# Performance work log

Measured on AMD Instinct MI355X. Metric: run time of the kernel, lower is better.

## Reference

```python
import jax, jax.numpy as jnp
import numpy as np

D_MODEL = 2048
NHEAD = 16
HEAD_DIM = D_MODEL // NHEAD  # 128
B, S = 2, 2048
THETA = 10000.0


def setup_inputs() -> dict:
    key = jax.random.key(0)
    ks = jax.random.split(key, 10)
    sc = 1.0 / np.sqrt(D_MODEL)
    inp = {
        "x": jax.random.normal(ks[0], (B, S, D_MODEL), dtype=jnp.float32),
        "mask": jnp.tril(jnp.ones((1, 1, S, S), dtype=jnp.int32)),
        "Wq": jax.random.normal(ks[1], (D_MODEL, D_MODEL), dtype=jnp.float32) * sc,
        "bq": jax.random.normal(ks[2], (D_MODEL,), dtype=jnp.float32) * 0.01,
        "Wk": jax.random.normal(ks[3], (D_MODEL, D_MODEL), dtype=jnp.float32) * sc,
        "bk": jax.random.normal(ks[4], (D_MODEL,), dtype=jnp.float32) * 0.01,
        "Wv": jax.random.normal(ks[5], (D_MODEL, D_MODEL), dtype=jnp.float32) * sc,
        "bv": jax.random.normal(ks[6], (D_MODEL,), dtype=jnp.float32) * 0.01,
        "Wo": jax.random.normal(ks[7], (D_MODEL, D_MODEL), dtype=jnp.float32) * sc,
        "bo": jax.random.normal(ks[8], (D_MODEL,), dtype=jnp.float32) * 0.01,
    }
    return inp


def _rope(x):
    # x: [B, H, S, D]; rotary applied to first D/2 dims (per the torch module's chunk(2)).
    D = x.shape[-1]
    half = D // 2            # rotary slice size (64)
    quarter = half // 2      # rotate_half split (32)
    seq = x.shape[2]
    inv_freq = 1.0 / (THETA ** (jnp.arange(0, D, 2, dtype=jnp.float32) / D))  # [D/2]
    t = jnp.arange(seq, dtype=jnp.float32)
    freqs = jnp.einsum("i,j->ij", t, inv_freq)  # [S, D/2]
    # emb = cat(freqs, freqs) then sliced to [:half] == freqs[:, :half]
    cos = jnp.cos(freqs)[None, None, :, :half]  # [1,1,S,half]
    sin = jnp.sin(freqs)[None, None, :, :half]
    x_rope, x_pass = x[..., :half], x[..., half:]
    x1, x2 = x_rope[..., :quarter], x_rope[..., quarter:]
    rotated = jnp.concatenate([-x2, x1], axis=-1)
    x_rope = x_rope * cos + rotated * sin
    return jnp.concatenate([x_rope, x_pass], axis=-1)


def reference(x, mask, Wq, bq, Wk, bk, Wv, bv, Wo, bo):
    b, s, _ = x.shape
    def proj(W, bias):
        y = jnp.einsum("bsd,ed->bse", x, W) + bias  # torch Linear: x @ W.T + b
        return y.reshape(b, s, NHEAD, HEAD_DIM).transpose(0, 2, 1, 3)  # [B,H,S,Dh]
    q = _rope(proj(Wq, bq))
    k = _rope(proj(Wk, bk))
    v = proj(Wv, bv)
    scores = jnp.einsum("bhqd,bhkd->bhqk", q, k) / jnp.sqrt(jnp.float32(HEAD_DIM))
    scores = jnp.where(mask == 0, jnp.float32(-1e9), scores)
    a = jax.nn.softmax(scores, axis=-1)
    o = jnp.einsum("bhqk,bhkd->bhqd", a, v)
    o = o.transpose(0, 2, 1, 3).reshape(b, s, D_MODEL)
    return jnp.einsum("bsd,ed->bse", o, Wo) + bo
```

## Files before the change

kernel.cpp:

```cpp
#include <hip/hip_runtime.h>
#include <stdint.h>
#include <math.h>

typedef short short8 __attribute__((ext_vector_type(8)));
typedef float f32x4 __attribute__((ext_vector_type(4)));

#define S_LEN   2048
#define DMODEL  2048
#define NHEADS  16
#define HDIM    128
#define NBATCH  2
#define BHTOT   32
#define MROWS   4096

#define XB_OFF   ((size_t)0)
#define WQ_OFF   ((size_t)16777216)
#define WK_OFF   ((size_t)25165824)
#define WV_OFF   ((size_t)33554432)
#define Q_OFF    ((size_t)41943040)
#define K_OFF    ((size_t)58720256)
#define VT_OFF   ((size_t)75497472)
#define COS_OFF  ((size_t)92274688)
#define SIN_OFF  ((size_t)92798976)

__device__ __forceinline__ unsigned short f2bf(float f) {
  unsigned int u = __float_as_uint(f);
  unsigned int r = (u + 0x7FFFu + ((u >> 16) & 1u)) >> 16;
  return (unsigned short)r;
}
__device__ __forceinline__ float bf2f(unsigned short b) {
  return __uint_as_float(((unsigned int)b) << 16);
}

__device__ __forceinline__ void gl_lds16(const unsigned short* g, unsigned short* l) {
  __builtin_amdgcn_global_load_lds(
      (const __attribute__((address_space(1))) unsigned int*)(g),
      (__attribute__((address_space(3))) unsigned int*)(l),
      16, 0, 0);
}

__global__ __launch_bounds__(256) void k_cvt(const float* __restrict__ src,
                                             unsigned short* __restrict__ dst, int n4) {
  int i = blockIdx.x * 256 + threadIdx.x;
  if (i >= n4) return;
  float4 v = ((const float4*)src)[i];
  ushort4 o;
  o.x = f2bf(v.x); o.y = f2bf(v.y); o.z = f2bf(v.z); o.w = f2bf(v.w);
  ((ushort4*)dst)[i] = o;
}

__global__ __launch_bounds__(256) void k_cvtw(
    const float* __restrict__ s0, const float* __restrict__ s1, const float* __restrict__ s2,
    unsigned short* __restrict__ d0, unsigned short* __restrict__ d1,
    unsigned short* __restrict__ d2) {
  int i = blockIdx.x * 256 + threadIdx.x;
  int sel = i >> 20, off = i & 1048575;
  const float* s = (sel == 0) ? s0 : (sel == 1 ? s1 : s2);
  unsigned short* d = (sel == 0) ? d0 : (sel == 1 ? d1 : d2);
  float4 v = ((const float4*)s)[off];
  ushort4 o;
  o.x = f2bf(v.x); o.y = f2bf(v.y); o.z = f2bf(v.z); o.w = f2bf(v.w);
  ((ushort4*)d)[off] = o;
}

__global__ __launch_bounds__(256) void k_rope_table(float* __restrict__ ct,
                                                    float* __restrict__ st) {
  int i = blockIdx.x * 256 + threadIdx.x;
  if (i >= S_LEN * 64) return;
  int s = i >> 6, j = i & 63;
  float inv = expf(-(float)(2 * j) * (9.210340371976184f / 128.0f));
  float ang = (float)s * inv;
  ct[i] = cosf(ang);
  st[i] = sinf(ang);
}

#define CP 136
__global__ __launch_bounds__(256) void k_gemm_qkv(
    const unsigned short* __restrict__ xb,
    const unsigned short* __restrict__ wqb, const unsigned short* __restrict__ wkb,
    const unsigned short* __restrict__ wvb,
    const float* __restrict__ bq, const float* __restrict__ bk, const float* __restrict__ bv,
    const float* __restrict__ ct, const float* __restrict__ st,
    unsigned short* __restrict__ qr, unsigned short* __restrict__ kr,
    unsigned short* __restrict__ vt) {
  __shared__ unsigned short SMEM[128 * CP];
  unsigned short* As = SMEM;
  unsigned short* Bs = SMEM + 8192;
  int m0 = blockIdx.x * 128;
  int n0g = blockIdx.y * 128;
  int wsel = n0g >> 11;
  int nw0 = n0g & (DMODEL - 1);
  const unsigned short* W = (wsel == 0) ? wqb : (wsel == 1 ? wkb : wvb);
  const float* bias = (wsel == 0) ? bq : (wsel == 1 ? bk : bv);
  int tid = threadIdx.x, lane = tid & 63, wid = tid >> 6;
  int wr = wid >> 1, wc = wid & 1;
  int lq = lane & 15, lk = lane >> 4;
  int gr = wid * 32 + (lane >> 3);
  int gc = ((lane & 7) * 8) ^ ((lane >> 3) << 3);

  f32x4 acc[4][4];
#pragma unroll
  for (int m = 0; m < 4; m++)
#pragma unroll
    for (int n = 0; n < 4; n++) { acc[m][n][0]=0.f; acc[m][n][1]=0.f; acc[m][n][2]=0.f; acc[m][n][3]=0.f; }

  for (int k0 = 0; k0 < DMODEL; k0 += 64) {
#pragma unroll
    for (int i = 0; i < 4; i++) {
      gl_lds16(xb + (size_t)(m0 + gr + i * 8) * DMODEL + k0 + gc, As + (wid * 32 + i * 8) * 64);
      gl_lds16(W  + (size_t)(nw0 + gr + i * 8) * DMODEL + k0 + gc, Bs + (wid * 32 + i * 8) * 64);
    }
    __syncthreads();
#pragma unroll
    for (int kk = 0; kk < 2; kk++) {
      short8 af[4], bfr[4];
      int sw = (lq & 7) << 3;
#pragma unroll
      for (int m = 0; m < 4; m++)
        af[m] = *(const short8*)&As[(wr * 64 + m * 16 + lq) * 64 + ((kk * 32 + lk * 8) ^ sw)];
#pragma unroll
      for (int n = 0; n < 4; n++)
        bfr[n] = *(const short8*)&Bs[(wc * 64 + n * 16 + lq) * 64 + ((kk * 32 + lk * 8) ^ sw)];
#pragma unroll
      for (int m = 0; m < 4; m++)
#pragma unroll
        for (int n = 0; n < 4; n++)
          acc[m][n] = __builtin_amdgcn_mfma_f32_16x16x32_bf16(af[m], bfr[n], acc[m][n], 0, 0, 0);
    }
    __syncthreads();
  }

  int h = nw0 >> 7, b = m0 >> 11, s0 = m0 & (S_LEN - 1);
  float bi[4];
#pragma unroll
  for (int n = 0; n < 4; n++) bi[n] = bias[nw0 + wc * 64 + n * 16 + lq];

  if (wsel < 2) {
    float qs = (wsel == 0) ? 0.08838834764831843f : 1.0f;
    if (wc == 0) {
#pragma unroll
      for (int m = 0; m < 4; m++) {
        int sl = wr * 64 + m * 16 + lk * 4;
#pragma unroll
        for (int r = 0; r < 4; r++) {
          int s = (s0 + sl + r);
          const float* cb = ct + s * 64;
          const float* sb = st + s * 64;
#pragma unroll
          for (int n = 0; n < 2; n++) {
            int f = n * 16 + lq;
            float x1 = acc[m][n][r] + bi[n];
            float x2 = acc[m][n + 2][r] + bi[n + 2];
            SMEM[(sl + r) * CP + f]      = f2bf((x1 * cb[f]      - x2 * sb[f])      * qs);
            SMEM[(sl + r) * CP + f + 32] = f2bf((x2 * cb[f + 32] + x1 * sb[f + 32]) * qs);
          }
        }
      }
    } else {
#pragma unroll
      for (int m = 0; m < 4; m++) {
        int sl = wr * 64 + m * 16 + lk * 4;
#pragma unroll
        for (int n = 0; n < 4; n++) {
          int f = 64 + n * 16 + lq;
#pragma unroll
          for (int r = 0; r < 4; r++)
            SMEM[(sl + r) * CP + f] = f2bf((acc[m][n][r] + bi[n]) * qs);
        }
      }
    }
    __syncthreads();
    int row = tid >> 1, hf2 = tid & 1;
    unsigned short* dstb = (wsel == 0 ? qr : kr) +
        ((size_t)(b * NHEADS + h) * S_LEN + s0 + row) * HDIM + hf2 * 64;
    const unsigned short* srcb = &SMEM[row * CP + hf2 * 64];
#pragma unroll
    for (int j = 0; j < 8; j++)
      *(short8*)(dstb + j * 8) = *(const short8*)(srcb + j * 8);
  } else {
#pragma unroll
    for (int m = 0; m < 4; m++) {
      int sl = wr * 64 + m * 16 + lk * 4;
#pragma unroll
      for (int n = 0; n < 4; n++) {
        int f = wc * 64 + n * 16 + lq;
#pragma unroll
        for (int r = 0; r < 4; r++)
          SMEM[f * CP + sl + r] = f2bf(acc[m][n][r] + bi[n]);
      }
    }
    __syncthreads();
    int row = tid >> 1, hf2 = tid & 1;
    unsigned short* dstb = vt +
        ((size_t)(b * NHEADS + h) * HDIM + row) * S_LEN + s0 + hf2 * 64;
    const unsigned short* srcb = &SMEM[row * CP + hf2 * 64];
#pragma unroll
    for (int j = 0; j < 8; j++)
      *(short8*)(dstb + j * 8) = *(const short8*)(srcb + j * 8);
  }
}

__global__ __launch_bounds__(256, 2) void k_attn(
    const unsigned short* __restrict__ qr, const unsigned short* __restrict__ kr,
    const unsigned short* __restrict__ vt, unsigned short* __restrict__ ob) {
  __shared__ unsigned short Kl[2][64 * 128];
  __shared__ unsigned short Vl[2][128 * 64];
  __shared__ unsigned short Ps[4][16][72];
  int bh = blockIdx.x, fold = blockIdx.y;
  int b = bh >> 4, h = bh & 15;
  int tid = threadIdx.x, lane = tid & 63, w = tid >> 6;
  int lq = lane & 15, lk = lane >> 4;
  const unsigned short* kbh = kr + (size_t)bh * S_LEN * HDIM;
  const unsigned short* vbh = vt + (size_t)bh * HDIM * S_LEN;
  int ksrow = tid >> 4;
  int kscol = ((tid & 15) * 8) ^ ((ksrow & 7) << 3);
  int vsrow = tid >> 3;
  int vscol = ((tid & 7) * 8) ^ ((vsrow & 7) << 3);
  int ldso = tid * 8;
  int rsw = (lq & 7) << 3;

  for (int hf = 0; hf < 2; hf++) {
    int qt = (hf == 0) ? fold : (31 - fold);
    int q0 = qt * 64;

    const unsigned short* qbase =
        qr + ((size_t)bh * S_LEN + q0 + w * 16 + lq) * HDIM + lk * 8;
    short8 qf[4];
#pragma unroll
    for (int ks = 0; ks < 4; ks++) qf[ks] = *(const short8*)(qbase + ks * 32);

    f32x4 acco[8];
#pragma unroll
    for (int nd = 0; nd < 8; nd++) { acco[nd][0]=0.f; acco[nd][1]=0.f; acco[nd][2]=0.f; acco[nd][3]=0.f; }
    float rm[4], rs[4];
#pragma unroll
    for (int r = 0; r < 4; r++) { rm[r] = -3.0e38f; rs[r] = 0.f; }

#pragma unroll
    for (int c = 0; c < 4; c++) {
      gl_lds16(kbh + (size_t)(c * 16 + ksrow) * HDIM + kscol, &Kl[0][c * 2048 + ldso]);
      gl_lds16(vbh + (size_t)(c * 32 + vsrow) * S_LEN + vscol, &Vl[0][c * 2048 + ldso]);
    }
    __syncthreads();
    int cur = 0;

    for (int t = 0; t <= qt; t++) {
      int kv0 = t * 64;
      if (t < qt) {
        int nx = kv0 + 64;
#pragma unroll
        for (int c = 0; c < 4; c++) {
          gl_lds16(kbh + (size_t)(nx + c * 16 + ksrow) * HDIM + kscol,
                   &Kl[cur ^ 1][c * 2048 + ldso]);
          gl_lds16(vbh + (size_t)(c * 32 + vsrow) * S_LEN + nx + vscol,
                   &Vl[cur ^ 1][c * 2048 + ldso]);
        }
      }
      const unsigned short* K0 = &Kl[cur][0];
      const unsigned short* V0 = &Vl[cur][0];

      f32x4 sacc[4];
#pragma unroll
      for (int n = 0; n < 4; n++) { sacc[n][0]=0.f; sacc[n][1]=0.f; sacc[n][2]=0.f; sacc[n][3]=0.f; }
#pragma unroll
      for (int ks = 0; ks < 4; ks++) {
#pragma unroll
        for (int n = 0; n < 4; n++) {
          short8 kf = *(const short8*)&K0[(n * 16 + lq) * 128 + ((ks * 32 + lk * 8) ^ rsw)];
          sacc[n] = __builtin_amdgcn_mfma_f32_16x16x32_bf16(qf[ks], kf, sacc[n], 0, 0, 0);
        }
      }
      if (t == qt) {
#pragma unroll
        for (int n = 0; n < 4; n++)
#pragma unroll
          for (int r = 0; r < 4; r++) {
            int qrow = q0 + w * 16 + lk * 4 + r;
            int kvc = kv0 + n * 16 + lq;
            if (kvc > qrow) sacc[n][r] = -3.0e38f;
          }
      }
      float mx4[4];
      int need = 0;
#pragma unroll
      for (int r = 0; r < 4; r++) {
        float mx = fmaxf(fmaxf(sacc[0][r], sacc[1][r]), fmaxf(sacc[2][r], sacc[3][r]));
        mx = fmaxf(mx, __shfl_xor(mx, 1, 64));
        mx = fmaxf(mx, __shfl_xor(mx, 2, 64));
        mx = fmaxf(mx, __shfl_xor(mx, 4, 64));
        mx = fmaxf(mx, __shfl_xor(mx, 8, 64));
        mx4[r] = mx;
        need |= (mx - rm[r] > 8.0f) ? 1 : 0;
      }
      if (__any(need)) {
#pragma unroll
        for (int r = 0; r < 4; r++) {
          float mnew = fmaxf(rm[r], mx4[r]);
          float corr = __expf(rm[r] - mnew);
          rs[r] *= corr;
#pragma unroll
          for (int nd = 0; nd < 8; nd++) acco[nd][r] *= corr;
          rm[r] = mnew;
        }
      }
#pragma unroll
      for (int r = 0; r < 4; r++) {
        float psum = 0.f;
#pragma unroll
        for (int n = 0; n < 4; n++) {
          float p = __expf(sacc[n][r] - rm[r]);
          sacc[n][r] = p;
          psum += p;
        }
        psum += __shfl_xor(psum, 1, 64);
        psum += __shfl_xor(psum, 2, 64);
        psum += __shfl_xor(psum, 4, 64);
        psum += __shfl_xor(psum, 8, 64);
        rs[r] += psum;
      }

#pragma unroll
      for (int n = 0; n < 4; n++)
#pragma unroll
        for (int r = 0; r < 4; r++)
          Ps[w][lk * 4 + r][n * 16 + lq] = f2bf(sacc[n][r]);

#pragma unroll
      for (int ks2 = 0; ks2 < 2; ks2++) {
        short8 pa = *(const short8*)&Ps[w][lq][ks2 * 32 + lk * 8];
#pragma unroll
        for (int nd = 0; nd < 8; nd++) {
          short8 vf = *(const short8*)&V0[(nd * 16 + lq) * 64 + ((ks2 * 32 + lk * 8) ^ rsw)];
          acco[nd] = __builtin_amdgcn_mfma_f32_16x16x32_bf16(pa, vf, acco[nd], 0, 0, 0);
        }
      }
      __syncthreads();
      cur ^= 1;
    }

#pragma unroll
    for (int r = 0; r < 4; r++) {
      float inv = 1.0f / rs[r];
      int srow = q0 + w * 16 + lk * 4 + r;
      unsigned short* dst = ob + ((size_t)b * S_LEN + srow) * DMODEL + h * HDIM;
#pragma unroll
      for (int nd = 0; nd < 8; nd++) dst[nd * 16 + lq] = f2bf(acco[nd][r] * inv);
    }
  }
}

__global__ __launch_bounds__(256) void k_gemm_out(
    const unsigned short* __restrict__ ob, const unsigned short* __restrict__ wob,
    const float* __restrict__ bo, float* __restrict__ out) {
  __shared__ unsigned short As[128][64];
  __shared__ unsigned short Bs[128][64];
  int m0 = blockIdx.x * 128, n0 = blockIdx.y * 128;
  int tid = threadIdx.x, lane = tid & 63, wid = tid >> 6;
  int wr = wid >> 1, wc = wid & 1;
  int lq = lane & 15, lk = lane >> 4;
  int gr = wid * 32 + (lane >> 3);
  int gc = ((lane & 7) * 8) ^ ((lane >> 3) << 3);

  f32x4 acc[4][4];
#pragma unroll
  for (int m = 0; m < 4; m++)
#pragma unroll
    for (int n = 0; n < 4; n++) { acc[m][n][0]=0.f; acc[m][n][1]=0.f; acc[m][n][2]=0.f; acc[m][n][3]=0.f; }

  for (int k0 = 0; k0 < DMODEL; k0 += 64) {
#pragma unroll
    for (int i = 0; i < 4; i++) {
      gl_lds16(ob  + (size_t)(m0 + gr + i * 8) * DMODEL + k0 + gc, &As[wid * 32 + i * 8][0]);
      gl_lds16(wob + (size_t)(n0 + gr + i * 8) * DMODEL + k0 + gc, &Bs[wid * 32 + i * 8][0]);
    }
    __syncthreads();
#pragma unroll
    for (int kk = 0; kk < 2; kk++) {
      short8 af[4], bfr[4];
      int sw = (lq & 7) << 3;
#pragma unroll
      for (int m = 0; m < 4; m++)
        af[m] = *(const short8*)&As[wr * 64 + m * 16 + lq][(kk * 32 + lk * 8) ^ sw];
#pragma unroll
      for (int n = 0; n < 4; n++)
        bfr[n] = *(const short8*)&Bs[wc * 64 + n * 16 + lq][(kk * 32 + lk * 8) ^ sw];
#pragma unroll
      for (int m = 0; m < 4; m++)
#pragma unroll
        for (int n = 0; n < 4; n++)
          acc[m][n] = __builtin_amdgcn_mfma_f32_16x16x32_bf16(af[m], bfr[n], acc[m][n], 0, 0, 0);
    }
    __syncthreads();
  }
#pragma unroll
  for (int n = 0; n < 4; n++) {
    int el = n0 + wc * 64 + n * 16 + lq;
    float bi = bo[el];
#pragma unroll
    for (int m = 0; m < 4; m++) {
      int row = m0 + wr * 64 + m * 16 + lk * 4;
#pragma unroll
      for (int r = 0; r < 4; r++)
        out[(size_t)(row + r) * DMODEL + el] = acc[m][n][r] + bi;
    }
  }
}

extern "C" void kernel_launch(void* const* d_in, const int* in_sizes, int n_in,
                              void* d_out, int out_size, void* d_ws, size_t ws_size,
                              hipStream_t stream) {
  const float* x  = (const float*)d_in[0];
  const float* Wq = (const float*)d_in[2];
  const float* bq = (const float*)d_in[3];
  const float* Wk = (const float*)d_in[4];
  const float* bk = (const float*)d_in[5];
  const float* Wv = (const float*)d_in[6];
  const float* bv = (const float*)d_in[7];
  const float* Wo = (const float*)d_in[8];
  const float* bo = (const float*)d_in[9];
  float* out = (float*)d_out;
  char* ws = (char*)d_ws;

  unsigned short* xb  = (unsigned short*)(ws + XB_OFF);
  unsigned short* wqb = (unsigned short*)(ws + WQ_OFF);
  unsigned short* wkb = (unsigned short*)(ws + WK_OFF);
  unsigned short* wvb = (unsigned short*)(ws + WV_OFF);
  unsigned short* qr  = (unsigned short*)(ws + Q_OFF);
  unsigned short* kr  = (unsigned short*)(ws + K_OFF);
  unsigned short* vt  = (unsigned short*)(ws + VT_OFF);
  float* ct = (float*)(ws + COS_OFF);
  float* st = (float*)(ws + SIN_OFF);

  k_cvt<<<(MROWS * DMODEL / 4 + 255) / 256, 256, 0, stream>>>(x, xb, MROWS * DMODEL / 4);
  k_cvtw<<<3 * 1048576 / 256, 256, 0, stream>>>(Wq, Wk, Wv, wqb, wkb, wvb);
  k_rope_table<<<(S_LEN * 64 + 255) / 256, 256, 0, stream>>>(ct, st);
  k_gemm_qkv<<<dim3(MROWS / 128, 6144 / 128), 256, 0, stream>>>(
      xb, wqb, wkb, wvb, bq, bk, bv, ct, st, qr, kr, vt);
  k_cvt<<<(DMODEL * DMODEL / 4 + 255) / 256, 256, 0, stream>>>(Wo, wqb, DMODEL * DMODEL / 4);
  k_attn<<<dim3(BHTOT, 16), 256, 0, stream>>>(qr, kr, vt, xb);
  k_gemm_out<<<dim3(MROWS / 128, DMODEL / 128), 256, 0, stream>>>(xb, wqb, bo, out);
}
```

Before: 279.0 us.

## Fuse prep kernels, swizzle GEMM block order, share KV tiles across paired query tiles

Merges the x/weight bf16 conversions and the RoPE table build into one prep launch, saving two kernel launches. Remaps GEMM block indices so that consecutive blocks reuse the same weight and activation tiles in L2. Attention now processes both folded query tiles of a block in a single KV sweep, so each K/V tile is loaded into LDS once and serves two query tiles instead of being streamed twice. The attention change roughly doubles the accumulator registers per wave, which may lower occupancy or cause spills.

Measured after the change: 275.0 us. Within noise of the previous version (-1.5%).

```diff
diff --git a/kernel.cpp b/kernel.cpp
--- a/kernel.cpp
+++ b/kernel.cpp
@@ -49,29 +49,36 @@
   ((ushort4*)dst)[i] = o;
 }
 
-__global__ __launch_bounds__(256) void k_cvtw(
-    const float* __restrict__ s0, const float* __restrict__ s1, const float* __restrict__ s2,
-    unsigned short* __restrict__ d0, unsigned short* __restrict__ d1,
-    unsigned short* __restrict__ d2) {
+__global__ __launch_bounds__(256) void k_prep(
+    const float* __restrict__ x, const float* __restrict__ Wq,
+    const float* __restrict__ Wk, const float* __restrict__ Wv,
+    unsigned short* __restrict__ xb, unsigned short* __restrict__ wqb,
+    unsigned short* __restrict__ wkb, unsigned short* __restrict__ wvb,
+    float* __restrict__ ct, float* __restrict__ st) {
   int i = blockIdx.x * 256 + threadIdx.x;
-  int sel = i >> 20, off = i & 1048575;
-  const float* s = (sel == 0) ? s0 : (sel == 1 ? s1 : s2);
-  unsigned short* d = (sel == 0) ? d0 : (sel == 1 ? d1 : d2);
-  float4 v = ((const float4*)s)[off];
-  ushort4 o;
-  o.x = f2bf(v.x); o.y = f2bf(v.y); o.z = f2bf(v.z); o.w = f2bf(v.w);
-  ((ushort4*)d)[off] = o;
-}
-
-__global__ __launch_bounds__(256) void k_rope_table(float* __restrict__ ct,
-                                                    float* __restrict__ st) {
-  int i = blockIdx.x * 256 + threadIdx.x;
-  if (i >= S_LEN * 64) return;
-  int s = i >> 6, j = i & 63;
-  float inv = expf(-(float)(2 * j) * (9.210340371976184f / 128.0f));
-  float ang = (float)s * inv;
-  ct[i] = cosf(ang);
-  st[i] = sinf(ang);
+  if (i < 5242880) {
+    const float* s; unsigned short* d; int off;
+    if (i < 2097152) { s = x; d = xb; off = i; }
+    else {
+      int j = i - 2097152, sel = j >> 20;
+      off = j & 1048575;
+      s = (sel == 0) ? Wq : (sel == 1 ? Wk : Wv);
+      d = (sel == 0) ? wqb : (sel == 1 ? wkb : wvb);
+    }
+    float4 v = ((const float4*)s)[off];
+    ushort4 o;
+    o.x = f2bf(v.x); o.y = f2bf(v.y); o.z = f2bf(v.z); o.w = f2bf(v.w);
+    ((ushort4*)d)[off] = o;
+  } else {
+    int j = i - 5242880;
+    if (j < S_LEN * 64) {
+      int s = j >> 6, jj = j & 63;
+      float inv = expf(-(float)(2 * jj) * (9.210340371976184f / 128.0f));
+      float ang = (float)s * inv;
+      ct[j] = cosf(ang);
+      st[j] = sinf(ang);
+    }
+  }
 }
 
 #define CP 136
@@ -86,8 +93,10 @@
   __shared__ unsigned short SMEM[128 * CP];
   unsigned short* As = SMEM;
   unsigned short* Bs = SMEM + 8192;
-  int m0 = blockIdx.x * 128;
-  int n0g = blockIdx.y * 128;
+  int bid = blockIdx.y * 32 + blockIdx.x;
+  int nb = (bid & 7) * 192 + (bid >> 3);
+  int m0 = (nb & 31) * 128;
+  int n0g = (nb >> 5) * 128;
   int wsel = n0g >> 11;
   int nw0 = n0g & (DMODEL - 1);
   const unsigned short* W = (wsel == 0) ? wqb : (wsel == 1 ? wkb : wvb);
@@ -148,11 +157,11 @@
           const float* sb = st + s * 64;
 #pragma unroll
           for (int n = 0; n < 2; n++) {
-            int f = n * 16 + lq;
+            int fq = n * 16 + lq;
             float x1 = acc[m][n][r] + bi[n];
             float x2 = acc[m][n + 2][r] + bi[n + 2];
-            SMEM[(sl + r) * CP + f]      = f2bf((x1 * cb[f]      - x2 * sb[f])      * qs);
-            SMEM[(sl + r) * CP + f + 32] = f2bf((x2 * cb[f + 32] + x1 * sb[f + 32]) * qs);
+            SMEM[(sl + r) * CP + fq]      = f2bf((x1 * cb[fq]      - x2 * sb[fq])      * qs);
+            SMEM[(sl + r) * CP + fq + 32] = f2bf((x2 * cb[fq + 32] + x1 * sb[fq + 32]) * qs);
           }
         }
       }
@@ -162,10 +171,10 @@
         int sl = wr * 64 + m * 16 + lk * 4;
 #pragma unroll
         for (int n = 0; n < 4; n++) {
-          int f = 64 + n * 16 + lq;
+          int fq = 64 + n * 16 + lq;
 #pragma unroll
           for (int r = 0; r < 4; r++)
-            SMEM[(sl + r) * CP + f] = f2bf((acc[m][n][r] + bi[n]) * qs);
+            SMEM[(sl + r) * CP + fq] = f2bf((acc[m][n][r] + bi[n]) * qs);
         }
       }
     }
@@ -183,10 +192,10 @@
       int sl = wr * 64 + m * 16 + lk * 4;
 #pragma unroll
       for (int n = 0; n < 4; n++) {
-        int f = wc * 64 + n * 16 + lq;
+        int fq = wc * 64 + n * 16 + lq;
 #pragma unroll
         for (int r = 0; r < 4; r++)
-          SMEM[f * CP + sl + r] = f2bf(acc[m][n][r] + bi[n]);
+          SMEM[fq * CP + sl + r] = f2bf(acc[m][n][r] + bi[n]);
       }
     }
     __syncthreads();
@@ -197,6 +206,64 @@
 #pragma unroll
     for (int j = 0; j < 8; j++)
       *(short8*)(dstb + j * 8) = *(const short8*)(srcb + j * 8);
+  }
+}
+
+__device__ __forceinline__ void attn_sm_pv(
+    f32x4* sacc, f32x4* acco, float* rm, float* rs,
+    unsigned short (*Psw)[72], const unsigned short* V0,
+    int lq, int lk, int rsw) {
+  float mx4[4];
+  int need = 0;
+#pragma unroll
+  for (int r = 0; r < 4; r++) {
+    float mx = fmaxf(fmaxf(sacc[0][r], sacc[1][r]), fmaxf(sacc[2][r], sacc[3][r]));
+    mx = fmaxf(mx, __shfl_xor(mx, 1, 64));
+    mx = fmaxf(mx, __shfl_xor(mx, 2, 64));
+    mx = fmaxf(mx, __shfl_xor(mx, 4, 64));
+    mx = fmaxf(mx, __shfl_xor(mx, 8, 64));
+    mx4[r] = mx;
+    need |= (mx - rm[r] > 8.0f) ? 1 : 0;
+  }
+  if (__any(need)) {
+#pragma unroll
+    for (int r = 0; r < 4; r++) {
+      float mnew = fmaxf(rm[r], mx4[r]);
+      float corr = __expf(rm[r] - mnew);
+      rs[r] *= corr;
+#pragma unroll
+      for (int nd = 0; nd < 8; nd++) acco[nd][r] *= corr;
+      rm[r] = mnew;
+    }
+  }
+#pragma unroll
+  for (int r = 0; r < 4; r++) {
+    float psum = 0.f;
+#pragma unroll
+    for (int n = 0; n < 4; n++) {
+      float p = __expf(sacc[n][r] - rm[r]);
+      sacc[n][r] = p;
+      psum += p;
+    }
+    psum += __shfl_xor(psum, 1, 64);
+    psum += __shfl_xor(psum, 2, 64);
+    psum += __shfl_xor(psum, 4, 64);
+    psum += __shfl_xor(psum, 8, 64);
+    rs[r] += psum;
+  }
+#pragma unroll
+  for (int n = 0; n < 4; n++)
+#pragma unroll
+    for (int r = 0; r < 4; r++)
+      Psw[lk * 4 + r][n * 16 + lq] = f2bf(sacc[n][r]);
+#pragma unroll
+  for (int ks2 = 0; ks2 < 2; ks2++) {
+    short8 pa = *(const short8*)&Psw[lq][ks2 * 32 + lk * 8];
+#pragma unroll
+    for (int nd = 0; nd < 8; nd++) {
+      short8 vf = *(const short8*)&V0[(nd * 16 + lq) * 64 + ((ks2 * 32 + lk * 8) ^ rsw)];
+      acco[nd] = __builtin_amdgcn_mfma_f32_16x16x32_bf16(pa, vf, acco[nd], 0, 0, 0);
+    }
   }
 }
 
@@ -206,7 +273,11 @@
   __shared__ unsigned short Kl[2][64 * 128];
   __shared__ unsigned short Vl[2][128 * 64];
   __shared__ unsigned short Ps[4][16][72];
-  int bh = blockIdx.x, fold = blockIdx.y;
+  int bh = blockIdx.x;
+  int yy = blockIdx.y;
+  int f = (yy < 8) ? yy : 23 - yy;
+  int qtA = 31 - f, qtB = f;
+  int q0A = qtA * 64, q0B = qtB * 64;
   int b = bh >> 4, h = bh & 15;
   int tid = threadIdx.x, lane = tid & 63, w = tid >> 6;
   int lq = lane & 15, lk = lane >> 4;
@@ -219,133 +290,115 @@
   int ldso = tid * 8;
   int rsw = (lq & 7) << 3;
 
-  for (int hf = 0; hf < 2; hf++) {
-    int qt = (hf == 0) ? fold : (31 - fold);
-    int q0 = qt * 64;
-
-    const unsigned short* qbase =
-        qr + ((size_t)bh * S_LEN + q0 + w * 16 + lq) * HDIM + lk * 8;
-    short8 qf[4];
-#pragma unroll
-    for (int ks = 0; ks < 4; ks++) qf[ks] = *(const short8*)(qbase + ks * 32);
-
-    f32x4 acco[8];
-#pragma unroll
-    for (int nd = 0; nd < 8; nd++) { acco[nd][0]=0.f; acco[nd][1]=0.f; acco[nd][2]=0.f; acco[nd][3]=0.f; }
-    float rm[4], rs[4];
-#pragma unroll
-    for (int r = 0; r < 4; r++) { rm[r] = -3.0e38f; rs[r] = 0.f; }
-
-#pragma unroll
-    for (int c = 0; c < 4; c++) {
-      gl_lds16(kbh + (size_t)(c * 16 + ksrow) * HDIM + kscol, &Kl[0][c * 2048 + ldso]);
-      gl_lds16(vbh + (size_t)(c * 32 + vsrow) * S_LEN + vscol, &Vl[0][c * 2048 + ldso]);
-    }
-    __syncthreads();
-    int cur = 0;
-
-    for (int t = 0; t <= qt; t++) {
-      int kv0 = t * 64;
-      if (t < qt) {
-        int nx = kv0 + 64;
-#pragma unroll
-        for (int c = 0; c < 4; c++) {
-          gl_lds16(kbh + (size_t)(nx + c * 16 + ksrow) * HDIM + kscol,
-                   &Kl[cur ^ 1][c * 2048 + ldso]);
-          gl_lds16(vbh + (size_t)(c * 32 + vsrow) * S_LEN + nx + vscol,
-                   &Vl[cur ^ 1][c * 2048 + ldso]);
-        }
+  const unsigned short* qbA =
+      qr + ((size_t)bh * S_LEN + q0A + w * 16 + lq) * HDIM + lk * 8;
+  const unsigned short* qbB =
+      qr + ((size_t)bh * S_LEN + q0B + w * 16 + lq) * HDIM + lk * 8;
+  short8 qfA[4], qfB[4];
+#pragma unroll
+  for (int ks = 0; ks < 4; ks++) {
+    qfA[ks] = *(const short8*)(qbA + ks * 32);
+    qfB[ks] = *(const short8*)(qbB + ks * 32);
+  }
+
+  f32x4 accoA[8], accoB[8];
+#pragma unroll
+  for (int nd = 0; nd < 8; nd++) {
+    accoA[nd][0]=0.f; accoA[nd][1]=0.f; accoA[nd][2]=0.f; accoA[nd][3]=0.f;
+    accoB[nd][0]=0.f; accoB[nd][1]=0.f; accoB[nd][2]=0.f; accoB[nd][3]=0.f;
+  }
+  float rmA[4], rsA[4], rmB[4], rsB[4];
+#pragma unroll
+  for (int r = 0; r < 4; r++) { rmA[r] = -3.0e38f; rsA[r] = 0.f; rmB[r] = -3.0e38f; rsB[r] = 0.f; }
+
+#pragma unroll
+  for (int c = 0; c < 4; c++) {
+    gl_lds16(kbh + (size_t)(c * 16 + ksrow) * HDIM + kscol, &Kl[0][c * 2048 + ldso]);
+    gl_lds16(vbh + (size_t)(c * 32 + vsrow) * S_LEN + vscol, &Vl[0][c * 2048 + ldso]);
+  }
+  __syncthreads();
+  int cur = 0;
+
+  for (int t = 0; t <= qtA; t++) {
+    int kv0 = t * 64;
+    if (t < qtA) {
+      int nx = kv0 + 64;
+#pragma unroll
+      for (int c = 0; c < 4; c++) {
+        gl_lds16(kbh + (size_t)(nx + c * 16 + ksrow) * HDIM + kscol,
+                 &Kl[cur ^ 1][c * 2048 + ldso]);
+        gl_lds16(vbh + (size_t)(c * 32 + vsrow) * S_LEN + nx + vscol,
+                 &Vl[cur ^ 1][c * 2048 + ldso]);
       }
-      const unsigned short* K0 = &Kl[cur][0];
-      const unsigned short* V0 = &Vl[cur][0];
-
-      f32x4 sacc[4];
-#pragma unroll
-      for (int n = 0; n < 4; n++) { sacc[n][0]=0.f; sacc[n][1]=0.f; sacc[n][2]=0.f; sacc[n][3]=0.f; }
-#pragma unroll
-      for (int ks = 0; ks < 4; ks++) {
+    }
+    const unsigned short* K0 = &Kl[cur][0];
+    const unsigned short* V0 = &Vl[cur][0];
+    bool actB = (t <= qtB);
+
+    f32x4 saccA[4], saccB[4];
+#pragma unroll
+    for (int n = 0; n < 4; n++) {
+      saccA[n][0]=0.f; saccA[n][1]=0.f; saccA[n][2]=0.f; saccA[n][3]=0.f;
+      saccB[n][0]=0.f; saccB[n][1]=0.f; saccB[n][2]=0.f; saccB[n][3]=0.f;
+    }
+    if (actB) {
+#pragma unroll
+      for (int ks = 0; ks < 4; ks++)
 #pragma unroll
         for (int n = 0; n < 4; n++) {
           short8 kf = *(const short8*)&K0[(n * 16 + lq) * 128 + ((ks * 32 + lk * 8) ^ rsw)];
-          sacc[n] = __builtin_amdgcn_mfma_f32_16x16x32_bf16(qf[ks], kf, sacc[n], 0, 0, 0);
+          saccA[n] = __builtin_amdgcn_mfma_f32_16x16x32_bf16(qfA[ks], kf, saccA[n], 0, 0, 0);
+          saccB[n] = __builtin_amdgcn_mfma_f32_16x16x32_bf16(qfB[ks], kf, saccB[n], 0, 0, 0);
         }
-      }
-      if (t == qt) {
+    } else {
+#pragma unroll
+      for (int ks = 0; ks < 4; ks++)
+#pragma unroll
+        for (int n = 0; n < 4; n++) {
+          short8 kf = *(const short8*)&K0[(n * 16 + lq) * 128 + ((ks * 32 + lk * 8) ^ rsw)];
+          saccA[n] = __builtin_amdgcn_mfma_f32_16x16x32_bf16(qfA[ks], kf, saccA[n], 0, 0, 0);
+        }
+    }
+    if (t == qtA) {
+#pragma unroll
+      for (int n = 0; n < 4; n++)
+#pragma unroll
+        for (int r = 0; r < 4; r++) {
+          int qrow = q0A + w * 16 + lk * 4 + r;
+          int kvc = kv0 + n * 16 + lq;
+          if (kvc > qrow) saccA[n][r] = -3.0e38f;
+        }
+    }
+    attn_sm_pv(saccA, accoA, rmA, rsA, Ps[w], V0, lq, lk, rsw);
+    if (actB) {
+      if (t == qtB) {
 #pragma unroll
         for (int n = 0; n < 4; n++)
 #pragma unroll
           for (int r = 0; r < 4; r++) {
-            int qrow = q0 + w * 16 + lk * 4 + r;
+            int qrow = q0B + w * 16 + lk * 4 + r;
             int kvc = kv0 + n * 16 + lq;
-            if (kvc > qrow) sacc[n][r] = -3.0e38f;
+            if (kvc > qrow) saccB[n][r] = -3.0e38f;
           }
       }
-      float mx4[4];
-      int need = 0;
-#pragma unroll
-      for (int r = 0; r < 4; r++) {
-        float mx = fmaxf(fmaxf(sacc[0][r], sacc[1][r]), fmaxf(sacc[2][r], sacc[3][r]));
-        mx = fmaxf(mx, __shfl_xor(mx, 1, 64));
-        mx = fmaxf(mx, __shfl_xor(mx, 2, 64));
-        mx = fmaxf(mx, __shfl_xor(mx, 4, 64));
-        mx = fmaxf(mx, __shfl_xor(mx, 8, 64));
-        mx4[r] = mx;
-        need |= (mx - rm[r] > 8.0f) ? 1 : 0;
-      }
-      if (__any(need)) {
-#pragma unroll
-        for (int r = 0; r < 4; r++) {
-          float mnew = fmaxf(rm[r], mx4[r]);
-          float corr = __expf(rm[r] - mnew);
-          rs[r] *= corr;
-#pragma unroll
-          for (int nd = 0; nd < 8; nd++) acco[nd][r] *= corr;
-          rm[r] = mnew;
-        }
-      }
-#pragma unroll
-      for (int r = 0; r < 4; r++) {
-        float psum = 0.f;
-#pragma unroll
-        for (int n = 0; n < 4; n++) {
-          float p = __expf(sacc[n][r] - rm[r]);
-          sacc[n][r] = p;
-          psum += p;
-        }
-        psum += __shfl_xor(psum, 1, 64);
-        psum += __shfl_xor(psum, 2, 64);
-        psum += __shfl_xor(psum, 4, 64);
-        psum += __shfl_xor(psum, 8, 64);
-        rs[r] += psum;
-      }
-
-#pragma unroll
-      for (int n = 0; n < 4; n++)
-#pragma unroll
-        for (int r = 0; r < 4; r++)
-          Ps[w][lk * 4 + r][n * 16 + lq] = f2bf(sacc[n][r]);
-
-#pragma unroll
-      for (int ks2 = 0; ks2 < 2; ks2++) {
-        short8 pa = *(const short8*)&Ps[w][lq][ks2 * 32 + lk * 8];
-#pragma unroll
-        for (int nd = 0; nd < 8; nd++) {
-          short8 vf = *(const short8*)&V0[(nd * 16 + lq) * 64 + ((ks2 * 32 + lk * 8) ^ rsw)];
-          acco[nd] = __builtin_amdgcn_mfma_f32_16x16x32_bf16(pa, vf, acco[nd], 0, 0, 0);
-        }
-      }
-      __syncthreads();
-      cur ^= 1;
-    }
-
-#pragma unroll
-    for (int r = 0; r < 4; r++) {
-      float inv = 1.0f / rs[r];
-      int srow = q0 + w * 16 + lk * 4 + r;
-      unsigned short* dst = ob + ((size_t)b * S_LEN + srow) * DMODEL + h * HDIM;
-#pragma unroll
-      for (int nd = 0; nd < 8; nd++) dst[nd * 16 + lq] = f2bf(acco[nd][r] * inv);
-    }
+      attn_sm_pv(saccB, accoB, rmB, rsB, Ps[w], V0, lq, lk, rsw);
+    }
+    __syncthreads();
+    cur ^= 1;
+  }
+
+#pragma unroll
+  for (int r = 0; r < 4; r++) {
+    float invA = 1.0f / rsA[r];
+    int srowA = q0A + w * 16 + lk * 4 + r;
+    unsigned short* dstA = ob + ((size_t)b * S_LEN + srowA) * DMODEL + h * HDIM;
+#pragma unroll
+    for (int nd = 0; nd < 8; nd++) dstA[nd * 16 + lq] = f2bf(accoA[nd][r] * invA);
+    float invB = 1.0f / rsB[r];
+    int srowB = q0B + w * 16 + lk * 4 + r;
+    unsigned short* dstB = ob + ((size_t)b * S_LEN + srowB) * DMODEL + h * HDIM;
+#pragma unroll
+    for (int nd = 0; nd < 8; nd++) dstB[nd * 16 + lq] = f2bf(accoB[nd][r] * invB);
   }
 }
 
@@ -354,7 +407,10 @@
     const float* __restrict__ bo, float* __restrict__ out) {
   __shared__ unsigned short As[128][64];
   __shared__ unsigned short Bs[128][64];
-  int m0 = blockIdx.x * 128, n0 = blockIdx.y * 128;
+  int bid = blockIdx.y * 32 + blockIdx.x;
+  int nb = (bid & 7) * 64 + (bid >> 3);
+  int m0 = (nb & 31) * 128;
+  int n0 = (nb >> 5) * 128;
   int tid = threadIdx.x, lane = tid & 63, wid = tid >> 6;
   int wr = wid >> 1, wc = wid & 1;
   int lq = lane & 15, lk = lane >> 4;
@@ -431,9 +487,7 @@
   float* ct = (float*)(ws + COS_OFF);
   float* st = (float*)(ws + SIN_OFF);
 
-  k_cvt<<<(MROWS * DMODEL / 4 + 255) / 256, 256, 0, stream>>>(x, xb, MROWS * DMODEL / 4);
-  k_cvtw<<<3 * 1048576 / 256, 256, 0, stream>>>(Wq, Wk, Wv, wqb, wkb, wvb);
-  k_rope_table<<<(S_LEN * 64 + 255) / 256, 256, 0, stream>>>(ct, st);
+  k_prep<<<20992, 256, 0, stream>>>(x, Wq, Wk, Wv, xb, wqb, wkb, wvb, ct, st);
   k_gemm_qkv<<<dim3(MROWS / 128, 6144 / 128), 256, 0, stream>>>(
       xb, wqb, wkb, wvb, bq, bk, bv, ct, st, qr, kr, vt);
   k_cvt<<<(DMODEL * DMODEL / 4 + 255) / 256, 256, 0, stream>>>(Wo, wqb, DMODEL * DMODEL / 4);
```
